# Kernel optimization log

Hardware: AMD Instinct MI355X
Metric: run time of the kernel (lower is better)

The kernel has to match this reference:

```python
import jax, jax.numpy as jnp
import numpy as np

COMMITMENT_COST = 0.25


def setup_inputs() -> dict:
    key = jax.random.key(0)
    k1, k2 = jax.random.split(key)
    N, K, D = 131072, 1024, 64
    inputs = jax.random.normal(k1, (N, D), dtype=jnp.float32)
    # torch init: uniform(-1/K, 1/K); use randn scaled similarly-small for a generic table
    embedding = jax.random.uniform(k2, (K, D), dtype=jnp.float32,
                                   minval=-1.0 / K, maxval=1.0 / K)
    return {"inputs": inputs, "embedding": embedding}


def reference(inputs, embedding):
    distances = (jnp.sum(inputs ** 2, axis=1, keepdims=True)
                 + jnp.sum(embedding ** 2, axis=1)
                 - 2.0 * inputs @ embedding.T)
    encoding_indices = jnp.argmin(distances, axis=1)            # [N]
    # direct gather (same math as one-hot @ embedding)
    quantized = embedding[encoding_indices]                     # [N, D]

    diff2 = jnp.mean((quantized - inputs) ** 2)
    # e_latent_loss == q_latent_loss numerically in fwd
    loss = diff2 + COMMITMENT_COST * diff2

    # straight-through output (forward value == quantized)
    quantized_st = inputs + jax.lax.stop_gradient(quantized - inputs)

    # avg_probs via histogram instead of materializing [N, K] one-hot
    N, K = inputs.shape[0], embedding.shape[0]
    counts = jnp.zeros((K,), dtype=jnp.float32).at[encoding_indices].add(1.0)
    avg_probs = counts / N
    perplexity = jnp.exp(-jnp.sum(avg_probs * jnp.log(avg_probs + 1e-10)))

    return quantized_st, loss, encoding_indices.reshape(N, 1), perplexity
```

## Files before the change

kernel.cpp:

```cpp
#include <hip/hip_runtime.h>
#include <hip/hip_bf16.h>

#define D 64
#define MARGIN 4e-5f
#define KS 4

typedef __attribute__((ext_vector_type(8))) short bf16x8;
typedef __attribute__((ext_vector_type(4))) float f32x4;
typedef __attribute__((ext_vector_type(4))) unsigned uint4v;


__device__ __forceinline__ float np_pairwise_sumsq64(const float* a) {
    float r[8];
#pragma unroll
    for (int j = 0; j < 8; ++j) r[j] = __fmul_rn(a[j], a[j]);
#pragma unroll
    for (int i = 8; i < 64; i += 8)
#pragma unroll
        for (int j = 0; j < 8; ++j)
            r[j] = __fadd_rn(r[j], __fmul_rn(a[i + j], a[i + j]));
    return __fadd_rn(
        __fadd_rn(__fadd_rn(r[0], r[1]), __fadd_rn(r[2], r[3])),
        __fadd_rn(__fadd_rn(r[4], r[5]), __fadd_rn(r[6], r[7])));
}

#define CVT8(F0, F1, H, L)                                                    \
    do {                                                                      \
        float _f[8] = {F0.x, F0.y, F0.z, F0.w, F1.x, F1.y, F1.z, F1.w};       \
        _Pragma("unroll") for (int _i = 0; _i < 8; ++_i) {                    \
            unsigned _u = __float_as_uint(_f[_i]);                            \
            unsigned _hb = (_u + 0x7fffu + ((_u >> 16) & 1u)) >> 16;          \
            float _hf = __uint_as_float(_hb << 16);                           \
            float _r = _f[_i] - _hf;                                          \
            unsigned _u2 = __float_as_uint(_r);                               \
            unsigned _lb = (_u2 + 0x7fffu + ((_u2 >> 16) & 1u)) >> 16;        \
            H[_i] = (short)_hb;                                               \
            L[_i] = (short)_lb;                                               \
        }                                                                     \
    } while (0)

__global__ __launch_bounds__(256) void vq_prep_all(
    const float* __restrict__ emb, int K,
    float* __restrict__ eenp, float* __restrict__ neh,
    unsigned short* __restrict__ ehs, float* __restrict__ eT,
    unsigned* __restrict__ counts, unsigned* __restrict__ done) {
    int b = blockIdx.x;
    if (b < 64) {
        int t = b * 256 + threadIdx.x;
        int tile = t >> 8, r = t & 255, s = r >> 6, l = r & 63;
        int sub = l & 15, grp = l >> 4;
        int k = tile * 16 + sub;
        int d0 = ((s & 1) << 5) + (grp << 3);
        const float* e = emb + (size_t)k * D + d0;
        float4 f0 = *(const float4*)e;
        float4 f1 = *(const float4*)(e + 4);
        bf16x8 h, lo;
        CVT8(f0, f1, h, lo);
        *(bf16x8*)(ehs + (size_t)t * 8) = (s >> 1) ? lo : h;
    } else if (b < 68) {
        int k = (b - 64) * 256 + threadIdx.x;
        float s = np_pairwise_sumsq64(emb + (size_t)k * D);
        eenp[k] = s;
        neh[k] = -0.5f * s;
    } else if (b < 324) {
        int t = (b - 68) * 256 + threadIdx.x;
        int d = t / K, k = t - d * K;
        eT[t] = emb[(size_t)k * D + d];
    } else {
#pragma unroll
        for (int i = 0; i < 4; ++i) {
            int c = threadIdx.x + 256 * i;
            if (c < K) counts[c] = 0u;
        }
        if (threadIdx.x == 0) *done = 0u;
    }
}

__global__ __launch_bounds__(256) void vq_screen(
    const float* __restrict__ x, const unsigned short* __restrict__ ehs,
    const float* __restrict__ neh, int N, int K,
    float* __restrict__ m1p, float* __restrict__ m2p, int* __restrict__ bip,
    float* __restrict__ xxp) {
    const int tid = threadIdx.x;
    const int lane = tid & 63;
    const int wid = tid >> 6;
    const int kslice = blockIdx.x & (KS - 1);
    const int rowblk = blockIdx.x >> 2;
    const int row0 = rowblk * 256 + wid * 64;
    const int sub = lane & 15, grp = lane >> 4;
    const int g4 = grp << 2;
    const int k0 = kslice * (K / KS);
    const int NT = (K / KS) >> 4;
    const int t0 = k0 >> 4;

    __shared__ __align__(16) unsigned short lds[2][2048];

    bf16x8 xh[4][2], xl[4][2];
    float xq[4];
#pragma unroll
    for (int rt = 0; rt < 4; ++rt) {
        xq[rt] = 0.f;
        const float* xrow = x + (((size_t)(row0 + (rt << 4) + sub)) << 6) + (grp << 3);
#pragma unroll
        for (int s = 0; s < 2; ++s) {
            float4 f0 = *(const float4*)(xrow + (s << 5));
            float4 f1 = *(const float4*)(xrow + (s << 5) + 4);
            xq[rt] = fmaf(f0.x, f0.x, xq[rt]); xq[rt] = fmaf(f0.y, f0.y, xq[rt]);
            xq[rt] = fmaf(f0.z, f0.z, xq[rt]); xq[rt] = fmaf(f0.w, f0.w, xq[rt]);
            xq[rt] = fmaf(f1.x, f1.x, xq[rt]); xq[rt] = fmaf(f1.y, f1.y, xq[rt]);
            xq[rt] = fmaf(f1.z, f1.z, xq[rt]); xq[rt] = fmaf(f1.w, f1.w, xq[rt]);
            CVT8(f0, f1, xh[rt][s], xl[rt][s]);
        }
    }
#pragma unroll
    for (int rt = 0; rt < 4; ++rt) {
        xq[rt] += __shfl_xor(xq[rt], 16);
        xq[rt] += __shfl_xor(xq[rt], 32);
    }

    float m1[4], m2[4];
    int bi[4];
#pragma unroll
    for (int rt = 0; rt < 4; ++rt) { m1[rt] = -3e38f; m2[rt] = -3e38f; bi[rt] = 0; }

    const unsigned short* sbase = ehs + ((size_t)t0 << 11);
    const int slot = (wid << 9) + (lane << 3);

    uint4v tmp = *(const uint4v*)(sbase + slot);
    *(uint4v*)&lds[0][slot] = tmp;
    __syncthreads();

    for (int t = 0; t < NT; ++t) {
        const int cur = t & 1;
        if (t + 1 < NT)
            tmp = *(const uint4v*)(sbase + ((size_t)(t + 1) << 11) + slot);

        f32x4 cb = *(const f32x4*)(neh + k0 + (t << 4) + g4);
        const bf16x8* L = (const bf16x8*)&lds[cur][0];
        bf16x8 a0 = L[lane];
        bf16x8 a1 = L[64 + lane];
        bf16x8 a2 = L[128 + lane];
        bf16x8 a3 = L[192 + lane];

        f32x4 acc[4];
#pragma unroll
        for (int rt = 0; rt < 4; ++rt)
            acc[rt] = __builtin_amdgcn_mfma_f32_16x16x32_bf16(a0, xh[rt][0], cb, 0, 0, 0);
#pragma unroll
        for (int rt = 0; rt < 4; ++rt)
            acc[rt] = __builtin_amdgcn_mfma_f32_16x16x32_bf16(a2, xh[rt][0], acc[rt], 0, 0, 0);
#pragma unroll
        for (int rt = 0; rt < 4; ++rt)
            acc[rt] = __builtin_amdgcn_mfma_f32_16x16x32_bf16(a0, xl[rt][0], acc[rt], 0, 0, 0);
#pragma unroll
        for (int rt = 0; rt < 4; ++rt)
            acc[rt] = __builtin_amdgcn_mfma_f32_16x16x32_bf16(a1, xh[rt][1], acc[rt], 0, 0, 0);
#pragma unroll
        for (int rt = 0; rt < 4; ++rt)
            acc[rt] = __builtin_amdgcn_mfma_f32_16x16x32_bf16(a3, xh[rt][1], acc[rt], 0, 0, 0);
#pragma unroll
        for (int rt = 0; rt < 4; ++rt)
            acc[rt] = __builtin_amdgcn_mfma_f32_16x16x32_bf16(a1, xl[rt][1], acc[rt], 0, 0, 0);

        int cbase = k0 + (t << 4) + g4;
#pragma unroll
        for (int rt = 0; rt < 4; ++rt) {
#pragma unroll
            for (int j = 0; j < 4; ++j) {
                float v = acc[rt][j];
                int c = cbase + j;
                bool tk = v > m1[rt];
                m2[rt] = fminf(fmaxf(v, m2[rt]), m1[rt]);
                m1[rt] = tk ? v : m1[rt];
                bi[rt] = tk ? c : bi[rt];
            }
        }

        if (t + 1 < NT)
            *(uint4v*)&lds[cur ^ 1][slot] = tmp;
        __syncthreads();
    }

#pragma unroll
    for (int rt = 0; rt < 4; ++rt) {
#pragma unroll
        for (int off = 16; off <= 32; off <<= 1) {
            float om1 = __shfl_xor(m1[rt], off);
            float om2 = __shfl_xor(m2[rt], off);
            int obi = __shfl_xor(bi[rt], off);
            bool take = (om1 > m1[rt]) || (om1 == m1[rt] && obi < bi[rt]);
            m2[rt] = fmaxf(fminf(om1, m1[rt]), fmaxf(om2, m2[rt]));
            m1[rt] = take ? om1 : m1[rt];
            bi[rt] = take ? obi : bi[rt];
        }
    }

    if (lane < 16) {
#pragma unroll
        for (int rt = 0; rt < 4; ++rt) {
            size_t idx = (size_t)kslice * N + row0 + (rt << 4) + lane;
            m1p[idx] = m1[rt];
            m2p[idx] = m2[rt];
            bip[idx] = bi[rt];
            if (kslice == 0) xxp[row0 + (rt << 4) + lane] = xq[rt];
        }
    }
}

__global__ __launch_bounds__(256) void vq_epilogue(
    const float* __restrict__ x, const float* __restrict__ emb,
    const float* __restrict__ eT, const float* __restrict__ eenp,
    const float* __restrict__ m1p, const float* __restrict__ m2p,
    const int* __restrict__ bip, const float* __restrict__ xxp, int N, int K,
    float* __restrict__ outq, float* __restrict__ outidx,
    double* __restrict__ lossA) {
    const int tid = threadIdx.x;
    const int rows0 = blockIdx.x * 64;
    __shared__ int sdec[64];
    __shared__ int samb[64];
    __shared__ int snamb;
    __shared__ float sxrow[64];
    __shared__ float swm[4];
    __shared__ int swi[4];

    double lacc = 0.0;

    if (tid < 64) {
        int r = rows0 + tid;
        float gm1 = m1p[r], gm2 = m2p[r];
        int gbi = bip[r];
#pragma unroll
        for (int s = 1; s < KS; ++s) {
            size_t idx = (size_t)s * N + r;
            float m1b = m1p[idx], m2b = m2p[idx];
            int bb = bip[idx];
            bool take = m1b > gm1;
            gm2 = fmaxf(fminf(gm1, m1b), fmaxf(gm2, m2b));
            gm1 = take ? m1b : gm1;
            gbi = take ? bb : gbi;
        }
        bool amb = 2.0f * (gm1 - gm2) < MARGIN;
        unsigned long long mask = __ballot(amb);
        int dec = gbi;
        double lpart = 0.0;
        if (amb) {
            int rank = __popcll(mask & ((1ull << tid) - 1ull));
            samb[rank] = tid;
            dec = -1;
        } else {
            outidx[r] = (float)dec;
            lpart = (double)(xxp[r] - 2.0f * gm1);
        }
        sdec[tid] = dec;
        if (tid == 0) snamb = __popcll(mask);
#pragma unroll
        for (int off = 32; off; off >>= 1) lpart += __shfl_down(lpart, off);
        if (tid == 0) lacc = lpart;
    }
    __syncthreads();

    const int namb = snamb;
    const int w = tid >> 6, l = tid & 63;
    const f32x4* eT4 = (const f32x4*)eT;
    for (int j = 0; j < namb; ++j) {
        int lr = samb[j];
        int row = rows0 + lr;
        if (tid < 64) sxrow[tid] = x[(size_t)row * D + tid];
        __syncthreads();
        float xx = np_pairwise_sumsq64(sxrow);
        f32x4 dt = (f32x4){0.f, 0.f, 0.f, 0.f};
#pragma unroll 8
        for (int d = 0; d < D; ++d) {
            f32x4 ev = eT4[(size_t)d * 256 + tid];
            float xv = sxrow[d];
            dt[0] = __fmaf_rn(xv, ev[0], dt[0]);
            dt[1] = __fmaf_rn(xv, ev[1], dt[1]);
            dt[2] = __fmaf_rn(xv, ev[2], dt[2]);
            dt[3] = __fmaf_rn(xv, ev[3], dt[3]);
        }
        float bm = 1e30f;
        int bi = 0;
#pragma unroll
        for (int jj = 0; jj < 4; ++jj) {
            int k = (tid << 2) + jj;
            float dist = __fsub_rn(__fadd_rn(xx, eenp[k]),
                                   __fmul_rn(2.0f, dt[jj]));
            if (dist < bm) { bm = dist; bi = k; }
        }
#pragma unroll
        for (int off = 1; off < 64; off <<= 1) {
            float ov = __shfl_xor(bm, off);
            int oi = __shfl_xor(bi, off);
            if (ov < bm || (ov == bm && oi < bi)) { bm = ov; bi = oi; }
        }
        if (l == 0) { swm[w] = bm; swi[w] = bi; }
        __syncthreads();
        if (tid == 0) {
            float fm = swm[0];
            int fi = swi[0];
#pragma unroll
            for (int ww = 1; ww < 4; ++ww) {
                float ov = swm[ww];
                int oi = swi[ww];
                if (ov < fm || (ov == fm && oi < fi)) { fm = ov; fi = oi; }
            }
            sdec[lr] = fi;
            outidx[row] = (float)fi;
            lacc += (double)fm;
        }
        __syncthreads();
    }
    if (tid == 0) lossA[blockIdx.x] = lacc;

    const int chunk = tid & 15, rl = tid >> 4;
#pragma unroll
    for (int p = 0; p < 4; ++p) {
        int lr = p * 16 + rl;
        int dp = sdec[lr];
        float4 ev = *(const float4*)(emb + (size_t)dp * D + chunk * 4);
        *(float4*)(outq + (size_t)(rows0 + lr) * D + chunk * 4) = ev;
    }
}

__global__ __launch_bounds__(256) void vq_histperp(
    const float* __restrict__ outidx, int N, int K,
    unsigned* __restrict__ counts, unsigned* __restrict__ done,
    const double* __restrict__ lossA, int nA,
    float* __restrict__ out_loss, float* __restrict__ out_perp) {
    __shared__ unsigned h[1024];
    __shared__ unsigned rank_s;
#pragma unroll
    for (int i = 0; i < 4; ++i) h[threadIdx.x + 256 * i] = 0;
    __syncthreads();
    int per = N / gridDim.x;
    int base = blockIdx.x * per;
    for (int i = threadIdx.x; i < per; i += 256) {
        int k = (int)outidx[base + i];
        atomicAdd(&h[k], 1u);
    }
    __syncthreads();
#pragma unroll
    for (int i = 0; i < 4; ++i) {
        int b = threadIdx.x + 256 * i;
        unsigned v = h[b];
        if (b < K && v) atomicAdd(counts + b, v);
    }
    __threadfence();
    if (threadIdx.x == 0) rank_s = atomicAdd(done, 1u);
    __syncthreads();
    if (rank_s == gridDim.x - 1) {
        double part = 0.0;
        for (int k = threadIdx.x; k < K; k += 256) {
            unsigned c = atomicAdd(counts + k, 0u);
            double p = (double)c / (double)N;
            part += p * log(p + 1e-10);
        }
        double lsum = 0.0;
        for (int i = threadIdx.x; i < nA; i += 256) lsum += lossA[i];
#pragma unroll
        for (int off = 32; off; off >>= 1) {
            part += __shfl_down(part, off);
            lsum += __shfl_down(lsum, off);
        }
        __shared__ double ls[4], ls2[4];
        if ((threadIdx.x & 63) == 0) {
            ls[threadIdx.x >> 6] = part;
            ls2[threadIdx.x >> 6] = lsum;
        }
        __syncthreads();
        if (threadIdx.x == 0) {
            double s = ls[0] + ls[1] + ls[2] + ls[3];
            double L = ls2[0] + ls2[1] + ls2[2] + ls2[3];
            *out_perp = (float)exp(-s);
            *out_loss = (float)(1.25 * (L / ((double)N * (double)D)));
        }
    }
}

extern "C" void kernel_launch(void* const* d_in, const int* in_sizes, int n_in,
                              void* d_out, int out_size, void* d_ws, size_t ws_size,
                              hipStream_t stream) {
    const float* x = (const float*)d_in[0];
    const float* emb = (const float*)d_in[1];
    int N = in_sizes[0] / D;
    int K = in_sizes[1] / D;

    float* outq = (float*)d_out;
    float* out_loss = outq + (size_t)N * D;
    float* outidx = out_loss + 1;
    float* out_perp = outidx + N;

    char* ws = (char*)d_ws;
    unsigned* counts = (unsigned*)ws;
    unsigned* done = (unsigned*)(ws + (size_t)K * 4);
    size_t off = (size_t)K * 4 + 16;
    float* neh = (float*)(ws + off);            off += (size_t)K * 4;
    float* eenp = (float*)(ws + off);           off += (size_t)K * 4;
    unsigned short* ehs = (unsigned short*)(ws + off);  off += (size_t)K * 256;
    float* eT = (float*)(ws + off);              off += (size_t)K * D * 4;
    float* m1p = (float*)(ws + off);             off += (size_t)KS * N * 4;
    float* m2p = (float*)(ws + off);             off += (size_t)KS * N * 4;
    int* bip = (int*)(ws + off);                 off += (size_t)KS * N * 4;
    float* xxp = (float*)(ws + off);             off += (size_t)N * 4;
    int nA = N / 64;
    double* lossA = (double*)(ws + off);         off += (size_t)nA * 8;

    vq_prep_all<<<325, 256, 0, stream>>>(emb, K, eenp, neh, ehs, eT,
                                         counts, done);
    vq_screen<<<(N / 256) * KS, 256, 0, stream>>>(x, ehs, neh, N, K,
                                                  m1p, m2p, bip, xxp);
    vq_epilogue<<<N / 64, 256, 0, stream>>>(x, emb, eT, eenp, m1p, m2p, bip,
                                            xxp, N, K, outq, outidx, lossA);
    vq_histperp<<<16, 256, 0, stream>>>(outidx, N, K, counts, done,
                                        lossA, nA, out_loss, out_perp);
}
```

Before: 170.2 us.

## Pack candidate index into score mantissa bits and halve K-slice split

Encodes the local codebook index into the low 9 mantissa bits of each score, so the running argmax becomes a plain fmaxf with no compare, select or separate index register. This cuts VALU work in the inner screening loop and the cross-lane reduction. The K split drops from 4 slices to 2 (512 codes per slice, matching the 9-bit index field), and the ambiguity margin is doubled to cover the precision lost by truncating the mantissa. The cost is more rows falling into the exact-fallback path, and fewer, longer blocks in the screen kernel.

```diff
diff --git a/kernel.cpp b/kernel.cpp
--- a/kernel.cpp
+++ b/kernel.cpp
@@ -2,8 +2,8 @@
 #include <hip/hip_bf16.h>
 
 #define D 64
-#define MARGIN 4e-5f
-#define KS 4
+#define MARGIN 8e-5f
+#define KS 2
 
 typedef __attribute__((ext_vector_type(8))) short bf16x8;
 typedef __attribute__((ext_vector_type(4))) float f32x4;
@@ -85,7 +85,7 @@
     const int lane = tid & 63;
     const int wid = tid >> 6;
     const int kslice = blockIdx.x & (KS - 1);
-    const int rowblk = blockIdx.x >> 2;
+    const int rowblk = blockIdx.x >> 1;
     const int row0 = rowblk * 256 + wid * 64;
     const int sub = lane & 15, grp = lane >> 4;
     const int g4 = grp << 2;
@@ -119,9 +119,8 @@
     }
 
     float m1[4], m2[4];
-    int bi[4];
-#pragma unroll
-    for (int rt = 0; rt < 4; ++rt) { m1[rt] = -3e38f; m2[rt] = -3e38f; bi[rt] = 0; }
+#pragma unroll
+    for (int rt = 0; rt < 4; ++rt) { m1[rt] = -3e38f; m2[rt] = -3e38f; }
 
     const unsigned short* sbase = ehs + ((size_t)t0 << 11);
     const int slot = (wid << 9) + (lane << 3);
@@ -162,17 +161,16 @@
         for (int rt = 0; rt < 4; ++rt)
             acc[rt] = __builtin_amdgcn_mfma_f32_16x16x32_bf16(a1, xl[rt][1], acc[rt], 0, 0, 0);
 
-        int cbase = k0 + (t << 4) + g4;
+        const int baset = 511 - (t << 4) - g4;
 #pragma unroll
         for (int rt = 0; rt < 4; ++rt) {
 #pragma unroll
             for (int j = 0; j < 4; ++j) {
-                float v = acc[rt][j];
-                int c = cbase + j;
-                bool tk = v > m1[rt];
-                m2[rt] = fminf(fmaxf(v, m2[rt]), m1[rt]);
-                m1[rt] = tk ? v : m1[rt];
-                bi[rt] = tk ? c : bi[rt];
+                unsigned pv = (__float_as_uint(acc[rt][j]) & 0xFFFFFE00u)
+                              | (unsigned)(baset - j);
+                float p = __uint_as_float(pv);
+                m2[rt] = fminf(fmaxf(p, m2[rt]), m1[rt]);
+                m1[rt] = fmaxf(p, m1[rt]);
             }
         }
 
@@ -187,11 +185,9 @@
         for (int off = 16; off <= 32; off <<= 1) {
             float om1 = __shfl_xor(m1[rt], off);
             float om2 = __shfl_xor(m2[rt], off);
-            int obi = __shfl_xor(bi[rt], off);
-            bool take = (om1 > m1[rt]) || (om1 == m1[rt] && obi < bi[rt]);
-            m2[rt] = fmaxf(fminf(om1, m1[rt]), fmaxf(om2, m2[rt]));
-            m1[rt] = take ? om1 : m1[rt];
-            bi[rt] = take ? obi : bi[rt];
+            float lo = fminf(m1[rt], om1);
+            m1[rt] = fmaxf(m1[rt], om1);
+            m2[rt] = fmaxf(lo, fmaxf(m2[rt], om2));
         }
     }
 
@@ -199,9 +195,10 @@
 #pragma unroll
         for (int rt = 0; rt < 4; ++rt) {
             size_t idx = (size_t)kslice * N + row0 + (rt << 4) + lane;
+            int local = 511 - (int)(__float_as_uint(m1[rt]) & 511u);
             m1p[idx] = m1[rt];
             m2p[idx] = m2[rt];
-            bip[idx] = bi[rt];
+            bip[idx] = k0 + local;
             if (kslice == 0) xxp[row0 + (rt << 4) + lane] = xq[rt];
         }
     }
@@ -235,8 +232,9 @@
             float m1b = m1p[idx], m2b = m2p[idx];
             int bb = bip[idx];
             bool take = m1b > gm1;
-            gm2 = fmaxf(fminf(gm1, m1b), fmaxf(gm2, m2b));
-            gm1 = take ? m1b : gm1;
+            float lo = fminf(gm1, m1b);
+            gm1 = fmaxf(gm1, m1b);
+            gm2 = fmaxf(lo, fmaxf(gm2, m2b));
             gbi = take ? bb : gbi;
         }
         bool amb = 2.0f * (gm1 - gm2) < MARGIN;
@@ -249,7 +247,8 @@
             dec = -1;
         } else {
             outidx[r] = (float)dec;
-            lpart = (double)(xxp[r] - 2.0f * gm1);
+            float gm1v = __uint_as_float(__float_as_uint(gm1) & 0xFFFFFE00u);
+            lpart = (double)(xxp[r] - 2.0f * gm1v);
         }
         sdec[tid] = dec;
         if (tid == 0) snamb = __popcll(mask);
```

Measured after the change: 194.4 us. +14.2%, slower.
